# Optimization experiments

Measured on AMD Instinct MI355X. Metric: run time of the kernel, lower is better.

The kernel has to match this reference:

```python
import jax, jax.numpy as jnp
from jax import lax
import numpy as np


def _conv(x, w, stride):
    # x: [B,C,D,H,W], w: [3,3,3,Cin,Cout]; kernel 3, pad 1 (matches SubMConv3d / SparseConv3d(3, s, padding=1))
    return lax.conv_general_dilated(x, w, (stride, stride, stride), [(1, 1)] * 3,
                                    dimension_numbers=('NCDHW', 'DHWIO', 'NCDHW'))


def _bn_relu(y, scale, shift, mask):
    # eval-mode BatchNorm folded to scale/shift, ReLU, then restrict to active sites
    return jnp.maximum(y * scale[None, :, None, None, None] + shift[None, :, None, None, None], 0.0) * mask


def _downsample_mask(m):
    # SparseConv3d(k=3, s=2, p=1): output site active iff any input in its 3x3x3 window is active
    return lax.reduce_window(m, -jnp.inf, lax.max, (1, 1, 3, 3, 3), (1, 1, 2, 2, 2),
                             [(0, 0), (0, 0), (1, 1), (1, 1), (1, 1)])


def setup_inputs() -> dict:
    key = jax.random.key(0)
    ks = jax.random.split(key, 40)
    B, D = 1, 128
    occ = jax.random.uniform(ks[0], (B, 1, D, D, D)) < 0.05
    x = jax.random.normal(ks[1], (B, 16, D, D, D), jnp.float32) * occ

    def w(k, ci, co):
        return jax.random.normal(k, (3, 3, 3, ci, co), jnp.float32) * (1.0 / np.sqrt(27.0 * ci))

    def sc(k, c):
        return jax.random.uniform(k, (c,), jnp.float32, 0.5, 1.5)

    def sh(k, c):
        return jax.random.normal(k, (c,), jnp.float32) * 0.1

    chans = [(16, 16), (16, 16), (16, 32), (32, 32), (32, 32), (32, 64), (64, 64), (64, 64), (64, 64)]
    names = ['w0a', 'w0b', 'wd0', 'w1a', 'w1b', 'wd1', 'w2a', 'w2b', 'w2c']
    d = {'x': x, 'mask': occ}
    i = 2
    for n, (ci, co) in zip(names, chans):
        d[n] = w(ks[i], ci, co)
        d['s' + n[1:]] = sc(ks[i + 1], co)
        d['b' + n[1:]] = sh(ks[i + 2], co)
        i += 3
    return d


def reference(x, mask, w0a, s0a, b0a, w0b, s0b, b0b, wd0, sd0, bd0,
              w1a, s1a, b1a, w1b, s1b, b1b, wd1, sd1, bd1,
              w2a, s2a, b2a, w2b, s2b, b2b, w2c, s2c, b2c):
    m0 = mask.astype(x.dtype)                       # active sites at full res [B,1,128,128,128]
    h = _bn_relu(_conv(x, w0a, 1), s0a, b0a, m0)    # conv0 (subm0)
    h = _bn_relu(_conv(h, w0b, 1), s0b, b0b, m0)
    m1 = _downsample_mask(m0)                       # down0 activity [B,1,64,64,64]
    h = _bn_relu(_conv(h, wd0, 2), sd0, bd0, m1)
    h = _bn_relu(_conv(h, w1a, 1), s1a, b1a, m1)    # conv1 (subm1)
    h = _bn_relu(_conv(h, w1b, 1), s1b, b1b, m1)
    m2 = _downsample_mask(m1)                       # down1 activity [B,1,32,32,32]
    h = _bn_relu(_conv(h, wd1, 2), sd1, bd1, m2)
    h = _bn_relu(_conv(h, w2a, 1), s2a, b2a, m2)    # conv2 (subm2)
    h = _bn_relu(_conv(h, w2b, 1), s2b, b2b, m2)
    h = _bn_relu(_conv(h, w2c, 1), s2c, b2c, m2)
    return h                                        # .dense() -> [B,64,32,32,32]
```

## Files before the change

### kernel.cpp

```cpp
#include <hip/hip_runtime.h>
#include <cstdint>

typedef unsigned short u16;
typedef unsigned int u32;
typedef unsigned char u8;
typedef unsigned long long u64;
typedef __attribute__((ext_vector_type(8))) short short8;
typedef __attribute__((ext_vector_type(4))) float f32x4;

#define CAP 131072

__device__ __forceinline__ float bf1(u16 v){ union{u32 i; float f;} c; c.i = ((u32)v) << 16; return c.f; }
__device__ __forceinline__ u16 f2bf(float f){
    union{float f; u32 i;} c; c.f = f; u32 i = c.i;
    return (u16)((i + 0x7FFFu + ((i >> 16) & 1u)) >> 16);
}

constexpr int ilog2c(int n){ return n <= 1 ? 0 : 1 + ilog2c(n / 2); }

struct PAll {
    const void* w[9];
    u32 wstart[10];
    int cin[9], cout[9], mode[9];
    const void* s[18];
};

__global__ void detect_k(const u16* __restrict__ s0a, u32* __restrict__ flag){
    if (threadIdx.x == 0){
        int ok = 1;
        #pragma unroll
        for (int i = 0; i < 8; i += 2){
            u16 v = s0a[i];
            if (v < 0x3F00u || v > 0x3FC0u) ok = 0;
        }
        flag[0] = ok ? 1u : 0u;
    }
}

__global__ __launch_bounds__(256)
void prep_k(PAll J, u16* __restrict__ FR, float* __restrict__ S,
            const u32* __restrict__ flag){
    const int gi = blockIdx.x * 256 + threadIdx.x;
    const int wtot = (int)J.wstart[9];
    if (gi < wtot){
        int j = 0;
        while (gi >= (int)J.wstart[j + 1]) ++j;
        const int i = gi - (int)J.wstart[j];
        const void* w = J.w[j];
        const int CIN = J.cin[j], COUT = J.cout[j];
        const int jj = i & 7;
        const int lane = (i >> 3) & 63;
        int rest = i >> 9;
        int src = -1;
        if (J.mode[j] == 0){
            const int KC = CIN >> 5, NT = COUT >> 4;
            const int nt = rest % NT; rest /= NT;
            const int kc = rest % KC; const int tap = rest / KC;
            const int k = kc * 32 + (lane >> 4) * 8 + jj;
            const int co = nt * 16 + (lane & 15);
            src = (tap * CIN + k) * COUT + co;
        } else if (J.mode[j] == 1){
            const int nt = rest & 1; const int pair = rest >> 1;
            const int kg = (lane >> 4) * 8 + jj;
            const int tap = pair * 2 + (kg >> 4);
            const int ci = kg & 15;
            const int co = nt * 16 + (lane & 15);
            if (tap < 27) src = (tap * 16 + ci) * 32 + co;
        } else {
            const int pair = rest;
            const int kg = (lane >> 4) * 8 + jj;
            const int tap = pair * 2 + (kg >> 4);
            const int ci = kg & 15;
            const int co = lane & 15;
            if (tap < 27) src = (tap * 16 + ci) * 16 + co;
        }
        float v = 0.f;
        if (src >= 0) v = flag[0] ? bf1(((const u16*)w)[src]) : ((const float*)w)[src];
        FR[gi] = f2bf(v);
    } else {
        const int i2 = gi - wtot;
        const int len[18] = {16,16,16,16,32,32,32,32,32,32,64,64,64,64,64,64,64,64};
        const int off[18] = {0,16,32,48,64,96,128,160,192,224,256,320,384,448,512,576,640,704};
        if (i2 < 768){
            int b = 0, base = 0;
            while (i2 >= base + len[b]) { base += len[b]; ++b; }
            const int t = i2 - base;
            const float v = flag[0] ? bf1(((const u16*)J.s[b])[t]) : ((const float*)J.s[b])[t];
            S[off[b] + t] = v;
        }
    }
}

__global__ __launch_bounds__(256)
void actmask_k(const void* __restrict__ xv, u64* __restrict__ bmask,
               u32* __restrict__ bcnt, const u32* __restrict__ flag){
    const int v = blockIdx.x * 256 + threadIdx.x;
    const size_t N = 2097152;
    u32 a = 0;
    if (flag[0]) {
        const u16* x = (const u16*)xv;
        #pragma unroll
        for (int c = 0; c < 16; ++c) a |= (u32)(x[(size_t)c * N + v]) & 0x7FFFu;
    } else {
        const u32* x = (const u32*)xv;
        #pragma unroll
        for (int c = 0; c < 16; ++c) a |= x[(size_t)c * N + v] & 0x7FFFFFFFu;
    }
    const u64 m = __ballot(a != 0);
    __shared__ u32 wc[4];
    const int lane = threadIdx.x & 63, wv = threadIdx.x >> 6;
    if (lane == 0) { bmask[v >> 6] = m; wc[wv] = (u32)__popcll(m); }
    __syncthreads();
    if (threadIdx.x == 0) bcnt[blockIdx.x] = wc[0] + wc[1] + wc[2] + wc[3];
}

__global__ __launch_bounds__(1024)
void aux_k(const u32* __restrict__ bcnt, u32* __restrict__ boff, u32* __restrict__ cnt,
           const u64* __restrict__ bmask, u8* __restrict__ m1){
    if (blockIdx.x == 0){
        __shared__ u32 lds[1024];
        const int t = threadIdx.x;
        u32 loc[8]; u32 s = 0;
        #pragma unroll
        for (int i = 0; i < 8; ++i){ loc[i] = s; s += bcnt[t * 8 + i]; }
        lds[t] = s;
        __syncthreads();
        u32 v = s;
        for (int d = 1; d < 1024; d <<= 1){
            u32 o = (t >= d) ? lds[t - d] : 0;
            __syncthreads();
            v += o; lds[t] = v;
            __syncthreads();
        }
        const u32 base = v - s;
        #pragma unroll
        for (int i = 0; i < 8; ++i) boff[t * 8 + i] = base + loc[i];
        if (t == 1023) cnt[0] = v;
    } else {
        const int v = (blockIdx.x - 1) * 1024 + threadIdx.x;
        const int xo = v & 63, yo = (v >> 6) & 63, zo = v >> 12;
        u32 a = 0;
        #pragma unroll
        for (int kz = 0; kz < 3; ++kz){ const int iz = 2*zo + kz - 1; if ((unsigned)iz >= 128u) continue;
          #pragma unroll
          for (int ky = 0; ky < 3; ++ky){ const int iy = 2*yo + ky - 1; if ((unsigned)iy >= 128u) continue;
            #pragma unroll
            for (int kx = 0; kx < 3; ++kx){ const int ix = 2*xo + kx - 1; if ((unsigned)ix >= 128u) continue;
              const int vv = (iz * 128 + iy) * 128 + ix;
              a |= (u32)((bmask[vv >> 6] >> (vv & 63)) & 1ull);
        }}}
        m1[v] = (u8)a;
    }
}

__global__ __launch_bounds__(256)
void scatter2m_k(const void* __restrict__ xv, const u64* __restrict__ bmask,
                 const u32* __restrict__ boff, int* __restrict__ idxmap,
                 int* __restrict__ alist, u16* __restrict__ f,
                 const u32* __restrict__ flag,
                 const u8* __restrict__ m1, u8* __restrict__ m2){
    if (blockIdx.x < 8192){
        const int v = blockIdx.x * 256 + threadIdx.x;
        const int lane = threadIdx.x & 63, wv = threadIdx.x >> 6;
        const u64 m = bmask[v >> 6];
        __shared__ u32 wc[4];
        if (lane == 0) wc[wv] = (u32)__popcll(m);
        __syncthreads();
        u32 wbase = 0;
        for (int i = 0; i < wv; ++i) wbase += wc[i];
        const bool act = (m >> lane) & 1ull;
        const u32 rank = (u32)__popcll(m & ((1ull << lane) - 1ull));
        int slot = -1;
        if (act){
            const u32 sl = boff[blockIdx.x] + wbase + rank;
            if (sl < CAP){
                slot = (int)sl;
                alist[slot] = v;
                if (flag[0]){
                    const u16* x = (const u16*)xv;
                    #pragma unroll
                    for (int c = 0; c < 16; ++c) f[(size_t)slot * 16 + c] = x[(size_t)c * 2097152 + v];
                } else {
                    const float* x = (const float*)xv;
                    #pragma unroll
                    for (int c = 0; c < 16; ++c) f[(size_t)slot * 16 + c] = f2bf(x[(size_t)c * 2097152 + v]);
                }
            }
        }
        idxmap[v] = slot;
    } else {
        const int v = (int)(blockIdx.x - 8192) * 256 + threadIdx.x;
        const int xo = v & 31, yo = (v >> 5) & 31, zo = v >> 10;
        u8 a = 0;
        #pragma unroll
        for (int kz = 0; kz < 3; ++kz){ const int iz = 2*zo + kz - 1; if ((unsigned)iz >= 64u) continue;
          #pragma unroll
          for (int ky = 0; ky < 3; ++ky){ const int iy = 2*yo + ky - 1; if ((unsigned)iy >= 64u) continue;
            #pragma unroll
            for (int kx = 0; kx < 3; ++kx){ const int ix = 2*xo + kx - 1; if ((unsigned)ix >= 64u) continue;
              a |= m1[((size_t)iz * 64 + iy) * 64 + ix];
        }}}
        m2[v] = a;
    }
}

__global__ __launch_bounds__(256)
void sconvm_k(const u16* __restrict__ fin, const int* __restrict__ idxmap,
              const int* __restrict__ alist, const u32* __restrict__ cnt,
              const u16* __restrict__ wf, const float* __restrict__ sc,
              const float* __restrict__ sh, u16* __restrict__ fout){
    const int n = min((int)cnt[0], CAP);
    const int j = blockIdx.x * 4 + (threadIdx.x >> 6);
    const int sbase = j * 16;
    if (sbase >= n) return;
    const int lane = threadIdx.x & 63;
    const int m = lane & 15, quad = lane >> 4;

    const int s = sbase + m;
    const int v = (s < n) ? alist[s] : -1;
    int xo = 0, yo = 0, zo = 0;
    if (v >= 0){ xo = v & 127; yo = (v >> 7) & 127; zo = v >> 14; }

    f32x4 acc = {0.f,0.f,0.f,0.f};
    #pragma unroll
    for (int p = 0; p < 14; ++p){
        const int tp = p * 2 + (quad >> 1);
        short8 a = {0,0,0,0,0,0,0,0};
        if (v >= 0 && tp < 27){
            const int kz = tp / 9, ky = (tp / 3) % 3, kx = tp % 3;
            const int iz = zo + kz - 1, iy = yo + ky - 1, ix = xo + kx - 1;
            if ((unsigned)iz < 128u && (unsigned)iy < 128u && (unsigned)ix < 128u){
                const int sn = idxmap[((size_t)iz * 128 + iy) * 128 + ix];
                if (sn >= 0) a = *(const short8*)(fin + (size_t)sn * 16 + (quad & 1) * 8);
            }
        }
        short8 b = *(const short8*)(wf + ((size_t)p * 64 + lane) * 8);
        acc = __builtin_amdgcn_mfma_f32_16x16x32_bf16(a, b, acc, 0, 0, 0);
    }

    const int co = lane & 15;
    const float scl = sc[co], shf = sh[co];
    #pragma unroll
    for (int r = 0; r < 4; ++r){
        const int srow = sbase + quad * 4 + r;
        if (srow < n){
            fout[(size_t)srow * 16 + co] = f2bf(fmaxf(acc[r] * scl + shf, 0.f));
        }
    }
}

__global__ __launch_bounds__(256)
void convd0m_k(const u16* __restrict__ fbuf, const int* __restrict__ idxmap,
               const u16* __restrict__ wf, const float* __restrict__ sc,
               const float* __restrict__ sh, const u8* __restrict__ mk,
               u16* __restrict__ out)
{
    const int wj = blockIdx.x * 4 + (threadIdx.x >> 6);
    const int lane = threadIdx.x & 63;
    const int m = lane & 15, quad = lane >> 4;
    const int xo_b = (wj & 3) * 16;
    const int yo = (wj >> 2) & 63;
    const int zo = wj >> 8;

    f32x4 acc0 = {0.f,0.f,0.f,0.f}, acc1 = {0.f,0.f,0.f,0.f};
    const int ix_m = (xo_b + m) * 2 - 1;

    #pragma unroll
    for (int p = 0; p < 14; ++p){
        const int tp = p * 2 + (quad >> 1);
        short8 a = {0,0,0,0,0,0,0,0};
        if (tp < 27){
            const int kz = tp / 9, ky = (tp / 3) % 3, kx = tp % 3;
            const int iz = 2*zo + kz - 1, iy = 2*yo + ky - 1, ix = ix_m + kx;
            if ((unsigned)iz < 128u && (unsigned)iy < 128u && (unsigned)ix < 128u){
                const int sn = idxmap[((size_t)iz * 128 + iy) * 128 + ix];
                if (sn >= 0) a = *(const short8*)(fbuf + (size_t)sn * 16 + (quad & 1) * 8);
            }
        }
        short8 b0 = *(const short8*)(wf + ((size_t)(p*2+0) * 64 + lane) * 8);
        short8 b1 = *(const short8*)(wf + ((size_t)(p*2+1) * 64 + lane) * 8);
        acc0 = __builtin_amdgcn_mfma_f32_16x16x32_bf16(a, b0, acc0, 0, 0, 0);
        acc1 = __builtin_amdgcn_mfma_f32_16x16x32_bf16(a, b1, acc1, 0, 0, 0);
    }

    const int vb = wj * 16 + quad * 4;
    const u32 m4 = *(const u32*)(mk + vb);
    const int n = lane & 15;
    #pragma unroll
    for (int nt = 0; nt < 2; ++nt){
        const int co = nt * 16 + n;
        const float s = sc[co], h = sh[co];
        const f32x4 acc = nt ? acc1 : acc0;
        #pragma unroll
        for (int r = 0; r < 4; ++r){
            float val = fmaxf(acc[r] * s + h, 0.f);
            val = ((m4 >> (8*r)) & 0xFFu) ? val : 0.f;
            out[(size_t)(vb + r) * 32 + co] = f2bf(val);
        }
    }
}

template<int DIN, int DOUT, int CIN, int COUT, int STRIDE, bool FINAL>
__global__ __launch_bounds__(256)
void mconv_k(const u16* __restrict__ in, const u16* __restrict__ wf,
             const float* __restrict__ sc, const float* __restrict__ sh,
             const u8* __restrict__ mk, void* __restrict__ out,
             const u32* __restrict__ flag)
{
    constexpr int KC = CIN / 32;
    constexpr int NT = COUT / 16;
    constexpr int XT = DOUT / 16;
    const int wj = blockIdx.x * 4 + (threadIdx.x >> 6);
    const int lane = threadIdx.x & 63;
    const int m = lane & 15, quad = lane >> 4;

    const int xo_b = (wj % XT) * 16;
    const int yo = (wj / XT) % DOUT;
    const int zo = wj / (XT * DOUT);

    f32x4 acc[NT];
    #pragma unroll
    for (int i = 0; i < NT; ++i) acc[i] = (f32x4){0.f,0.f,0.f,0.f};

    const int ix0 = (xo_b + m) * STRIDE - 1;
    for (int kz = 0; kz < 3; ++kz){
      const int iz = zo * STRIDE + kz - 1;
      if ((unsigned)iz >= (unsigned)DIN) continue;
      for (int ky = 0; ky < 3; ++ky){
        const int iy = yo * STRIDE + ky - 1;
        if ((unsigned)iy >= (unsigned)DIN) continue;
        const size_t rowb = ((size_t)iz * DIN + iy) * DIN;
        #pragma unroll
        for (int kx = 0; kx < 3; ++kx){
          const int ix = ix0 + kx;
          const bool v = (unsigned)ix < (unsigned)DIN;
          const int tap = (kz*3 + ky)*3 + kx;
          const u16* ap = in + (rowb + ix) * CIN + quad * 8;
          const u16* bp = wf + (size_t)tap * KC * NT * 512 + lane * 8;
          #pragma unroll
          for (int kc = 0; kc < KC; ++kc){
            short8 a = {0,0,0,0,0,0,0,0};
            if (v) a = *(const short8*)(ap + kc * 32);
            #pragma unroll
            for (int nt = 0; nt < NT; ++nt){
              short8 b = *(const short8*)(bp + (kc * NT + nt) * 512);
              acc[nt] = __builtin_amdgcn_mfma_f32_16x16x32_bf16(a, b, acc[nt], 0, 0, 0);
            }
          }
    }}}

    const int vb = wj * 16 + quad * 4;
    const u32 m4 = *(const u32*)(mk + vb);
    const int n = lane & 15;
    #pragma unroll
    for (int nt = 0; nt < NT; ++nt){
        const int co = nt * 16 + n;
        const float s = sc[co], h = sh[co];
        #pragma unroll
        for (int r = 0; r < 4; ++r){
            float val = fmaxf(acc[nt][r] * s + h, 0.f);
            val = ((m4 >> (8*r)) & 0xFFu) ? val : 0.f;
            ((u16*)out)[(size_t)(vb + r) * COUT + co] = f2bf(val);
        }
    }
    (void)flag;
}

template<int D, int CIN, int COUT, bool FINAL>
__global__ __launch_bounds__((D/16)*2*64)
void mconvlds2_k(const u16* __restrict__ in, const u16* __restrict__ wf,
                 const float* __restrict__ sc, const float* __restrict__ sh,
                 const u8* __restrict__ mk, void* __restrict__ out,
                 const u32* __restrict__ flag)
{
    constexpr int KC = CIN / 32;
    constexpr int NT = COUT / 16;
    constexpr int CH8 = CIN / 8;
    constexpr int WPR = D / 16;
    constexpr int BT = WPR * 2 * 64;
    __shared__ u16 tile[12 * 2048];

    const int t = threadIdx.x;
    const int yo0 = (blockIdx.x % (D / 2)) * 2;
    const int zo  = blockIdx.x / (D / 2);

    #pragma unroll
    for (int ri = 0; ri < 12; ++ri){
        const int dz = ri >> 2, jy = ri & 3;
        const int iz = zo + dz - 1, iy = yo0 + jy - 1;
        if ((unsigned)iz < (unsigned)D && (unsigned)iy < (unsigned)D){
            const u16* src = in + ((size_t)(iz * D + iy) * D) * CIN;
            u16* dst = &tile[ri * 2048];
            for (int c = t; c < D * CH8; c += BT){
                const int x = c / CH8, c8 = c % CH8;
                *(short8*)(dst + (c8 * D + x) * 8) = *(const short8*)(src + c * 8);
            }
        }
    }
    __syncthreads();

    const int lane = t & 63, w = t >> 6;
    const int r2 = w / WPR;
    const int xo_b = (w % WPR) * 16;
    const int yo = yo0 + r2;
    const int m = lane & 15, quad = lane >> 4;

    f32x4 acc[NT];
    #pragma unroll
    for (int i = 0; i < NT; ++i) acc[i] = (f32x4){0.f,0.f,0.f,0.f};

    #pragma unroll
    for (int kz = 0; kz < 3; ++kz){
      const int iz = zo + kz - 1;
      if ((unsigned)iz >= (unsigned)D) continue;
      #pragma unroll
      for (int ky = 0; ky < 3; ++ky){
        const int iy = yo + ky - 1;
        if ((unsigned)iy >= (unsigned)D) continue;
        const u16* row = &tile[(kz * 4 + (r2 + ky)) * 2048];
        #pragma unroll
        for (int kx = 0; kx < 3; ++kx){
          const int ix = xo_b + m + kx - 1;
          const bool aok = (unsigned)ix < (unsigned)D;
          const int tap = (kz * 3 + ky) * 3 + kx;
          const u16* bp = wf + (size_t)tap * KC * NT * 512 + lane * 8;
          #pragma unroll
          for (int kc = 0; kc < KC; ++kc){
            short8 a = {0,0,0,0,0,0,0,0};
            if (aok) a = *(const short8*)(row + ((kc * 4 + quad) * D + ix) * 8);
            #pragma unroll
            for (int nt = 0; nt < NT; ++nt){
              short8 b = *(const short8*)(bp + (kc * NT + nt) * 512);
              acc[nt] = __builtin_amdgcn_mfma_f32_16x16x32_bf16(a, b, acc[nt], 0, 0, 0);
            }
          }
        }
      }
    }

    const int vb = (zo * D + yo) * D + xo_b + quad * 4;
    const u32 m4 = *(const u32*)(mk + vb);
    const int n = lane & 15;
    if (FINAL) {
        const bool bfout = flag[0] != 0;
        #pragma unroll
        for (int nt = 0; nt < NT; ++nt){
            const int co = nt * 16 + n;
            const float s = sc[co], h = sh[co];
            float4 o;
            float* po = &o.x;
            #pragma unroll
            for (int r = 0; r < 4; ++r){
                float val = fmaxf(acc[nt][r] * s + h, 0.f);
                po[r] = ((m4 >> (8*r)) & 0xFFu) ? val : 0.f;
            }
            if (!bfout) {
                *(float4*)((float*)out + (size_t)co * (D*D*D) + vb) = o;
            } else {
                u16* ob = (u16*)out + (size_t)co * (D*D*D) + vb;
                #pragma unroll
                for (int r = 0; r < 4; ++r) ob[r] = f2bf(po[r]);
            }
        }
    } else {
        #pragma unroll
        for (int nt = 0; nt < NT; ++nt){
            const int co = nt * 16 + n;
            const float s = sc[co], h = sh[co];
            #pragma unroll
            for (int r = 0; r < 4; ++r){
                float val = fmaxf(acc[nt][r] * s + h, 0.f);
                val = ((m4 >> (8*r)) & 0xFFu) ? val : 0.f;
                ((u16*)out)[(size_t)(vb + r) * COUT + co] = f2bf(val);
            }
        }
    }
}

extern "C" void kernel_launch(void* const* d_in, const int* in_sizes, int n_in,
                              void* d_out, int out_size, void* d_ws, size_t ws_size,
                              hipStream_t stream)
{
    (void)out_size; (void)ws_size;

    int wb = 2;
    for (int i = 1; i < n_in; ++i) { if (in_sizes[i] == 6912) { wb = i; break; } }

    const void* x = d_in[0];
    const void *w0a=d_in[wb+0],  *s0a=d_in[wb+1],  *b0a=d_in[wb+2];
    const void *w0b=d_in[wb+3],  *s0b=d_in[wb+4],  *b0b=d_in[wb+5];
    const void *wd0=d_in[wb+6],  *sd0=d_in[wb+7],  *bd0=d_in[wb+8];
    const void *w1a=d_in[wb+9],  *s1a=d_in[wb+10], *b1a=d_in[wb+11];
    const void *w1b=d_in[wb+12], *s1b=d_in[wb+13], *b1b=d_in[wb+14];
    const void *wd1=d_in[wb+15], *sd1=d_in[wb+16], *bd1=d_in[wb+17];
    const void *w2a=d_in[wb+18], *s2a=d_in[wb+19], *b2a=d_in[wb+20];
    const void *w2b=d_in[wb+21], *s2b=d_in[wb+22], *b2b=d_in[wb+23];
    const void *w2c=d_in[wb+24], *s2c=d_in[wb+25], *b2c=d_in[wb+26];

    char* ws = (char*)d_ws;
    int*   idxmap = (int*)(ws);
    u16*   Fb0    = (u16*)(ws + 8388608);
    u16*   Fb1    = (u16*)(ws + 12582912);
    u16*   Fb2    = (u16*)(ws + 16777216);
    u16*   Rb1    = (u16*)(ws + 25165824);
    u16*   Rb2    = (u16*)(ws + 41943040);
    u8*    m1     = (u8*)(ws + 58720256);
    u8*    m2     = (u8*)(ws + 58982400);
    u32*   cnt    = (u32*)(ws + 59015168);
    int*   alist  = (int*)(ws + 59015424);
    u16*   FR     = (u16*)(ws + 59539712);
    float* S      = (float*)(ws + 60483328);
    u32*   flag   = (u32*)(ws + 60486400);
    u64*   bmask  = (u64*)(ws + 60486656);
    u32*   bcnt   = (u32*)(ws + 60748800);
    u32*   boff   = (u32*)(ws + 60781568);

    u16* wfs0a = FR + 0;
    u16* wfs0b = FR + 7168;
    u16* fd0   = FR + 14336;
    u16* f1a   = FR + 28672;
    u16* f1b   = FR + 56320;
    u16* fd1   = FR + 83968;
    u16* f2a   = FR + 139264;
    u16* f2b   = FR + 249856;
    u16* f2c   = FR + 360448;

    detect_k<<<1, 64, 0, stream>>>((const u16*)s0a, flag);

    PAll J;
    const void* jsrc[9] = {w0a, w0b, wd0, w1a, w1b, wd1, w2a, w2b, w2c};
    const u32 jlen[9]   = {7168,7168,14336,27648,27648,55296,110592,110592,110592};
    const int jcin[9]   = {16,16,16,32,32,32,64,64,64};
    const int jcout[9]  = {16,16,32,32,32,64,64,64,64};
    const int jmode[9]  = {2,2,1,0,0,0,0,0,0};
    u32 acc = 0;
    for (int i = 0; i < 9; ++i){
        J.w[i] = jsrc[i]; J.wstart[i] = acc; acc += jlen[i];
        J.cin[i] = jcin[i]; J.cout[i] = jcout[i]; J.mode[i] = jmode[i];
    }
    J.wstart[9] = acc;
    const void* sv[18] = {s0a,b0a,s0b,b0b,sd0,bd0,s1a,b1a,s1b,b1b,sd1,bd1,s2a,b2a,s2b,b2b,s2c,b2c};
    for (int i = 0; i < 18; ++i) J.s[i] = sv[i];
    const u32 ptot = acc + 768;
    prep_k<<<(int)((ptot + 255) / 256), 256, 0, stream>>>(J, FR, S, flag);

    float *cs0a=S+0,  *cb0a=S+16,  *cs0b=S+32,  *cb0b=S+48;
    float *csd0=S+64, *cbd0=S+96,  *cs1a=S+128, *cb1a=S+160, *cs1b=S+192, *cb1b=S+224;
    float *csd1=S+256,*cbd1=S+320, *cs2a=S+384, *cb2a=S+448, *cs2b=S+512, *cb2b=S+576, *cs2c=S+640, *cb2c=S+704;

    actmask_k<<<8192, 256, 0, stream>>>(x, bmask, bcnt, flag);
    aux_k<<<257, 1024, 0, stream>>>(bcnt, boff, cnt, bmask, m1);
    scatter2m_k<<<8320, 256, 0, stream>>>(x, bmask, boff, idxmap, alist, Fb0, flag, m1, m2);

    sconvm_k<<<2048, 256, 0, stream>>>(Fb0, idxmap, alist, cnt, wfs0a, cs0a, cb0a, Fb1);
    sconvm_k<<<2048, 256, 0, stream>>>(Fb1, idxmap, alist, cnt, wfs0b, cs0b, cb0b, Fb2);
    convd0m_k<<<4096, 256, 0, stream>>>(Fb2, idxmap, fd0, csd0, cbd0, m1, Rb1);
    mconvlds2_k<64,32,32,false><<<2048, 512, 0, stream>>>(Rb1, f1a, cs1a, cb1a, m1, Rb2, flag);
    mconvlds2_k<64,32,32,false><<<2048, 512, 0, stream>>>(Rb2, f1b, cs1b, cb1b, m1, Rb1, flag);
    mconv_k<64,32,32,64,2,false><<<512, 256, 0, stream>>>(Rb1, fd1, csd1, cbd1, m2, Rb2, flag);
    mconvlds2_k<32,64,64,false><<<512, 256, 0, stream>>>(Rb2, f2a, cs2a, cb2a, m2, Rb1, flag);
    mconvlds2_k<32,64,64,false><<<512, 256, 0, stream>>>(Rb1, f2b, cs2b, cb2b, m2, Rb2, flag);
    mconvlds2_k<32,64,64,true ><<<512, 256, 0, stream>>>(Rb2, f2c, cs2c, cb2c, m2, d_out, flag);
}
```

Measured before the change: 511.4 us.

## Tile dense subm convs as 2x2 z-y output blocks and fold dtype detect into prep

Each dense submanifold conv block now computes a 2x2 patch of output rows over z and y instead of two y rows. Its LDS halo tile grows from 12 to 16 input rows and is shared by four output rows, which cuts redundant global loads per output. Block size doubles and grid size halves, and the larger LDS footprint may lower occupancy. The separate dtype-detection kernel is removed: every prep thread checks the scale values itself and thread 0 writes the flag, saving one launch.

```diff
diff --git a/kernel.cpp b/kernel.cpp
--- a/kernel.cpp
+++ b/kernel.cpp
@@ -25,22 +25,19 @@
     const void* s[18];
 };
 
-__global__ void detect_k(const u16* __restrict__ s0a, u32* __restrict__ flag){
-    if (threadIdx.x == 0){
-        int ok = 1;
-        #pragma unroll
-        for (int i = 0; i < 8; i += 2){
-            u16 v = s0a[i];
-            if (v < 0x3F00u || v > 0x3FC0u) ok = 0;
-        }
-        flag[0] = ok ? 1u : 0u;
-    }
-}
-
 __global__ __launch_bounds__(256)
 void prep_k(PAll J, u16* __restrict__ FR, float* __restrict__ S,
-            const u32* __restrict__ flag){
+            const u16* __restrict__ s0a_probe, u32* __restrict__ flag){
+    int ok = 1;
+    #pragma unroll
+    for (int i = 0; i < 8; i += 2){
+        u16 v = s0a_probe[i];
+        if (v < 0x3F00u || v > 0x3FC0u) ok = 0;
+    }
+    const u32 isbf = ok ? 1u : 0u;
     const int gi = blockIdx.x * 256 + threadIdx.x;
+    if (gi == 0) flag[0] = isbf;
+
     const int wtot = (int)J.wstart[9];
     if (gi < wtot){
         int j = 0;
@@ -75,7 +72,7 @@
             if (tap < 27) src = (tap * 16 + ci) * 16 + co;
         }
         float v = 0.f;
-        if (src >= 0) v = flag[0] ? bf1(((const u16*)w)[src]) : ((const float*)w)[src];
+        if (src >= 0) v = isbf ? bf1(((const u16*)w)[src]) : ((const float*)w)[src];
         FR[gi] = f2bf(v);
     } else {
         const int i2 = gi - wtot;
@@ -85,7 +82,7 @@
             int b = 0, base = 0;
             while (i2 >= base + len[b]) { base += len[b]; ++b; }
             const int t = i2 - base;
-            const float v = flag[0] ? bf1(((const u16*)J.s[b])[t]) : ((const float*)J.s[b])[t];
+            const float v = isbf ? bf1(((const u16*)J.s[b])[t]) : ((const float*)J.s[b])[t];
             S[off[b] + t] = v;
         }
     }
@@ -367,8 +364,8 @@
 }
 
 template<int D, int CIN, int COUT, bool FINAL>
-__global__ __launch_bounds__((D/16)*2*64)
-void mconvlds2_k(const u16* __restrict__ in, const u16* __restrict__ wf,
+__global__ __launch_bounds__((D/16)*4*64)
+void mconvlds4_k(const u16* __restrict__ in, const u16* __restrict__ wf,
                  const float* __restrict__ sc, const float* __restrict__ sh,
                  const u8* __restrict__ mk, void* __restrict__ out,
                  const u32* __restrict__ flag)
@@ -377,17 +374,17 @@
     constexpr int NT = COUT / 16;
     constexpr int CH8 = CIN / 8;
     constexpr int WPR = D / 16;
-    constexpr int BT = WPR * 2 * 64;
-    __shared__ u16 tile[12 * 2048];
+    constexpr int BT = WPR * 4 * 64;
+    __shared__ u16 tile[16 * 2048];
 
     const int t = threadIdx.x;
-    const int yo0 = (blockIdx.x % (D / 2)) * 2;
-    const int zo  = blockIdx.x / (D / 2);
-
-    #pragma unroll
-    for (int ri = 0; ri < 12; ++ri){
+    const int yp = blockIdx.x % (D / 2);
+    const int zp = blockIdx.x / (D / 2);
+
+    #pragma unroll
+    for (int ri = 0; ri < 16; ++ri){
         const int dz = ri >> 2, jy = ri & 3;
-        const int iz = zo + dz - 1, iy = yo0 + jy - 1;
+        const int iz = 2*zp + dz - 1, iy = 2*yp + jy - 1;
         if ((unsigned)iz < (unsigned)D && (unsigned)iy < (unsigned)D){
             const u16* src = in + ((size_t)(iz * D + iy) * D) * CIN;
             u16* dst = &tile[ri * 2048];
@@ -400,9 +397,10 @@
     __syncthreads();
 
     const int lane = t & 63, w = t >> 6;
-    const int r2 = w / WPR;
+    const int r = w / WPR;
+    const int r2z = r >> 1, r2y = r & 1;
     const int xo_b = (w % WPR) * 16;
-    const int yo = yo0 + r2;
+    const int zo = 2*zp + r2z, yo = 2*yp + r2y;
     const int m = lane & 15, quad = lane >> 4;
 
     f32x4 acc[NT];
@@ -417,7 +415,7 @@
       for (int ky = 0; ky < 3; ++ky){
         const int iy = yo + ky - 1;
         if ((unsigned)iy >= (unsigned)D) continue;
-        const u16* row = &tile[(kz * 4 + (r2 + ky)) * 2048];
+        const u16* row = &tile[((r2z + kz) * 4 + (r2y + ky)) * 2048];
         #pragma unroll
         for (int kx = 0; kx < 3; ++kx){
           const int ix = xo_b + m + kx - 1;
@@ -450,16 +448,16 @@
             float4 o;
             float* po = &o.x;
             #pragma unroll
-            for (int r = 0; r < 4; ++r){
-                float val = fmaxf(acc[nt][r] * s + h, 0.f);
-                po[r] = ((m4 >> (8*r)) & 0xFFu) ? val : 0.f;
+            for (int r4 = 0; r4 < 4; ++r4){
+                float val = fmaxf(acc[nt][r4] * s + h, 0.f);
+                po[r4] = ((m4 >> (8*r4)) & 0xFFu) ? val : 0.f;
             }
             if (!bfout) {
                 *(float4*)((float*)out + (size_t)co * (D*D*D) + vb) = o;
             } else {
                 u16* ob = (u16*)out + (size_t)co * (D*D*D) + vb;
                 #pragma unroll
-                for (int r = 0; r < 4; ++r) ob[r] = f2bf(po[r]);
+                for (int r4 = 0; r4 < 4; ++r4) ob[r4] = f2bf(po[r4]);
             }
         }
     } else {
@@ -468,10 +466,10 @@
             const int co = nt * 16 + n;
             const float s = sc[co], h = sh[co];
             #pragma unroll
-            for (int r = 0; r < 4; ++r){
-                float val = fmaxf(acc[nt][r] * s + h, 0.f);
-                val = ((m4 >> (8*r)) & 0xFFu) ? val : 0.f;
-                ((u16*)out)[(size_t)(vb + r) * COUT + co] = f2bf(val);
+            for (int r4 = 0; r4 < 4; ++r4){
+                float val = fmaxf(acc[nt][r4] * s + h, 0.f);
+                val = ((m4 >> (8*r4)) & 0xFFu) ? val : 0.f;
+                ((u16*)out)[(size_t)(vb + r4) * COUT + co] = f2bf(val);
             }
         }
     }
@@ -525,8 +523,6 @@
     u16* f2b   = FR + 249856;
     u16* f2c   = FR + 360448;
 
-    detect_k<<<1, 64, 0, stream>>>((const u16*)s0a, flag);
-
     PAll J;
     const void* jsrc[9] = {w0a, w0b, wd0, w1a, w1b, wd1, w2a, w2b, w2c};
     const u32 jlen[9]   = {7168,7168,14336,27648,27648,55296,110592,110592,110592};
@@ -542,7 +538,7 @@
     const void* sv[18] = {s0a,b0a,s0b,b0b,sd0,bd0,s1a,b1a,s1b,b1b,sd1,bd1,s2a,b2a,s2b,b2b,s2c,b2c};
     for (int i = 0; i < 18; ++i) J.s[i] = sv[i];
     const u32 ptot = acc + 768;
-    prep_k<<<(int)((ptot + 255) / 256), 256, 0, stream>>>(J, FR, S, flag);
+    prep_k<<<(int)((ptot + 255) / 256), 256, 0, stream>>>(J, FR, S, (const u16*)s0a, flag);
 
     float *cs0a=S+0,  *cb0a=S+16,  *cs0b=S+32,  *cb0b=S+48;
     float *csd0=S+64, *cbd0=S+96,  *cs1a=S+128, *cb1a=S+160, *cs1b=S+192, *cb1b=S+224;
@@ -555,10 +551,10 @@
     sconvm_k<<<2048, 256, 0, stream>>>(Fb0, idxmap, alist, cnt, wfs0a, cs0a, cb0a, Fb1);
     sconvm_k<<<2048, 256, 0, stream>>>(Fb1, idxmap, alist, cnt, wfs0b, cs0b, cb0b, Fb2);
     convd0m_k<<<4096, 256, 0, stream>>>(Fb2, idxmap, fd0, csd0, cbd0, m1, Rb1);
-    mconvlds2_k<64,32,32,false><<<2048, 512, 0, stream>>>(Rb1, f1a, cs1a, cb1a, m1, Rb2, flag);
-    mconvlds2_k<64,32,32,false><<<2048, 512, 0, stream>>>(Rb2, f1b, cs1b, cb1b, m1, Rb1, flag);
+    mconvlds4_k<64,32,32,false><<<1024, 1024, 0, stream>>>(Rb1, f1a, cs1a, cb1a, m1, Rb2, flag);
+    mconvlds4_k<64,32,32,false><<<1024, 1024, 0, stream>>>(Rb2, f1b, cs1b, cb1b, m1, Rb1, flag);
     mconv_k<64,32,32,64,2,false><<<512, 256, 0, stream>>>(Rb1, fd1, csd1, cbd1, m2, Rb2, flag);
-    mconvlds2_k<32,64,64,false><<<512, 256, 0, stream>>>(Rb2, f2a, cs2a, cb2a, m2, Rb1, flag);
-    mconvlds2_k<32,64,64,false><<<512, 256, 0, stream>>>(Rb1, f2b, cs2b, cb2b, m2, Rb2, flag);
-    mconvlds2_k<32,64,64,true ><<<512, 256, 0, stream>>>(Rb2, f2c, cs2c, cb2c, m2, d_out, flag);
-}
+    mconvlds4_k<32,64,64,false><<<256, 512, 0, stream>>>(Rb2, f2a, cs2a, cb2a, m2, Rb1, flag);
+    mconvlds4_k<32,64,64,false><<<256, 512, 0, stream>>>(Rb1, f2b, cs2b, cb2b, m2, Rb2, flag);
+    mconvlds4_k<32,64,64,true ><<<256, 512, 0, stream>>>(Rb2, f2c, cs2c, cb2c, m2, d_out, flag);
+}
```

New measurement: 511.0 us. Within noise of the previous version (-0.1%).
